# Optimization experiments

Measured on AMD Instinct MI355X. Metric: run time of the kernel, lower is better.

## Reference

```python
import jax, jax.numpy as jnp
import numpy as np

V, C = 100000, 400000          # variables, clauses
IN, OUT, H = 96, 64, 4         # in_channels, out_channels, heads
E_HALF = 1000000               # edges per direction
NEG_SLOPE = 0.2
LN_EPS = 1e-5


def _w(k, shape, fan_in):
    return (jax.random.normal(k, shape, jnp.float32) / np.sqrt(fan_in)).astype(jnp.float32)


def setup_inputs() -> dict:
    key = jax.random.key(0)
    ks = jax.random.split(key, 30)
    x = jax.random.normal(ks[0], (V + C, IN), jnp.float32)
    node_type = jnp.concatenate([jnp.full((V,), 1.0, jnp.float32), jnp.full((C,), 2.0, jnp.float32)])
    x = x.at[:, 0].set(node_type)  # NODE_TYPE_VAR=1, NODE_TYPE_CLAUSE=2
    # first half: "v2c" edges (source id >= num_vars), second half: "c2v" edges
    src1 = jax.random.randint(ks[1], (E_HALF,), V, 2 * V)   # -V -> index into x_var
    dst1 = jax.random.randint(ks[2], (E_HALF,), 0, C)       # index into x_clause
    src2 = jax.random.randint(ks[3], (E_HALF,), 0, V)       # index into h_c_new (V<=C so valid)
    dst2 = jax.random.randint(ks[4], (E_HALF,), V, 2 * V)   # -V -> index into x_var
    edge_index = jnp.stack([jnp.concatenate([src1, src2]),
                            jnp.concatenate([dst1, dst2])]).astype(jnp.int32)
    HD = H * OUT
    return {
        "x": x, "edge_index": edge_index, "num_vars": V,
        # v2c GATv2Conv (src=vars IN, dst=clauses IN)
        "v2c_Wl": _w(ks[5], (IN, HD), IN), "v2c_Wr": _w(ks[6], (IN, HD), IN),
        "v2c_att": _w(ks[7], (H, OUT), OUT), "v2c_bias": jnp.zeros((HD,), jnp.float32),
        "c_ln_g": jnp.ones((HD,), jnp.float32), "c_ln_b": jnp.zeros((HD,), jnp.float32),
        "c_Wih": _w(ks[8], (3 * OUT, HD), HD), "c_Whh": _w(ks[9], (3 * OUT, OUT), OUT),
        "c_bih": jnp.zeros((3 * OUT,), jnp.float32), "c_bhh": jnp.zeros((3 * OUT,), jnp.float32),
        # c2v GATv2Conv (src=clauses OUT, dst=vars IN)
        "c2v_Wl": _w(ks[10], (OUT, HD), OUT), "c2v_Wr": _w(ks[11], (IN, HD), IN),
        "c2v_att": _w(ks[12], (H, OUT), OUT), "c2v_bias": jnp.zeros((HD,), jnp.float32),
        "v_ln_g": jnp.ones((HD,), jnp.float32), "v_ln_b": jnp.zeros((HD,), jnp.float32),
        "v_Wih": _w(ks[13], (3 * OUT, HD), HD), "v_Whh": _w(ks[14], (3 * OUT, OUT), OUT),
        "v_bih": jnp.zeros((3 * OUT,), jnp.float32), "v_bhh": jnp.zeros((3 * OUT,), jnp.float32),
    }


def gatv2(x_src, x_dst, edge_index, Wl, Wr, att, bias, num_dst):
    """PyG GATv2Conv, concat=True, no self loops, eval mode (no attn dropout)."""
    h, d = att.shape
    xl = (x_src @ Wl).reshape(-1, h, d)   # [Ns, H, D]
    xr = (x_dst @ Wr).reshape(-1, h, d)   # [Nd, H, D]
    j, i = edge_index[0], edge_index[1]
    e = jax.nn.leaky_relu(xl[j] + xr[i], NEG_SLOPE)          # [E, H, D]
    alpha = jnp.einsum('ehd,hd->eh', e, att)                 # [E, H]
    amax = jax.ops.segment_max(alpha, i, num_segments=num_dst)
    alpha = jnp.exp(alpha - amax[i])
    denom = jax.ops.segment_sum(alpha, i, num_segments=num_dst)
    alpha = alpha / (denom[i] + 1e-16)
    msg = xl[j] * alpha[..., None]                           # [E, H, D]
    out = jax.ops.segment_sum(msg, i, num_segments=num_dst)  # [num_dst, H, D]
    return out.reshape(num_dst, h * d) + bias


def layernorm(x, g, b):
    mu = jnp.mean(x, axis=-1, keepdims=True)
    var = jnp.mean((x - mu) ** 2, axis=-1, keepdims=True)
    return (x - mu) * jax.lax.rsqrt(var + LN_EPS) * g + b


def gru_cell(x, hprev, Wih, Whh, bih, bhh):
    gi = x @ Wih.T + bih      # [N, 3*OUT]
    gh = hprev @ Whh.T + bhh  # [N, 3*OUT]
    ir, iz, inn = jnp.split(gi, 3, axis=-1)
    hr, hz, hn = jnp.split(gh, 3, axis=-1)
    r = jax.nn.sigmoid(ir + hr)
    z = jax.nn.sigmoid(iz + hz)
    n = jnp.tanh(inn + r * hn)
    return (1.0 - z) * n + z * hprev


def reference(x, edge_index, num_vars,
              v2c_Wl, v2c_Wr, v2c_att, v2c_bias, c_ln_g, c_ln_b,
              c_Wih, c_Whh, c_bih, c_bhh,
              c2v_Wl, c2v_Wr, c2v_att, c2v_bias, v_ln_g, v_ln_b,
              v_Wih, v_Whh, v_bih, v_bhh):
    out_ch = c_Whh.shape[1]
    n_nodes = x.shape[0]
    n_cla = n_nodes - num_vars
    h_old = x[:, -out_ch:]
    x_var, x_cla = x[:num_vars], x[num_vars:]           # vars first, clauses after
    h_v_old, h_c_old = h_old[:num_vars], h_old[num_vars:]
    e_half = edge_index.shape[1] // 2
    # edges with edge_index[0] >= num_vars (first half by construction), shift row 0
    v2c = jnp.stack([edge_index[0, :e_half] - num_vars, edge_index[1, :e_half]])
    m_c = gatv2(x_var, x_cla, v2c, v2c_Wl, v2c_Wr, v2c_att, v2c_bias, n_cla)
    m_c = layernorm(m_c, c_ln_g, c_ln_b)                # dropout = identity (eval)
    h_c_new = gru_cell(m_c, h_c_old, c_Wih, c_Whh, c_bih, c_bhh)
    # edges with edge_index[0] < num_vars (second half), shift row 1
    c2v = jnp.stack([edge_index[0, e_half:], edge_index[1, e_half:] - num_vars])
    m_v = gatv2(h_c_new, x_var, c2v, c2v_Wl, c2v_Wr, c2v_att, c2v_bias, num_vars)
    m_v = layernorm(m_v, v_ln_g, v_ln_b)
    h_v_new = gru_cell(m_v, h_v_old, v_Wih, v_Whh, v_bih, v_bhh)
    # x_new[var_mask]=h_v_new; x_new[clause_mask]=h_c_new (vars-first layout)
    return jnp.concatenate([h_v_new, h_c_new], axis=0)
```

## Files before the change

### kernel.cpp

```cpp
#include <hip/hip_runtime.h>
#include <hip/hip_bf16.h>
#include <cstdint>
#include <cstddef>

constexpr int V_NODES = 100000;
constexpr float NEG = 0.2f;
constexpr float LN_EPS = 1e-5f;
typedef __hip_bfloat16 bf16;

typedef __attribute__((ext_vector_type(8))) short short8v;
typedef __attribute__((ext_vector_type(4))) float f32x4;

__device__ inline float bflo(unsigned u){ return __uint_as_float(u << 16); }
__device__ inline float bfhi(unsigned u){ return __uint_as_float(u & 0xffff0000u); }
__device__ inline unsigned short f2bu(float x){ bf16 h = __float2bfloat16(x); return *reinterpret_cast<unsigned short*>(&h); }
__device__ inline unsigned bfpk(float x, float y){ return (unsigned)f2bu(x) | ((unsigned)f2bu(y) << 16); }

__device__ inline f32x4 mfma16(short8v a, short8v b, f32x4 c){
  return __builtin_amdgcn_mfma_f32_16x16x32_bf16(a, b, c, 0, 0, 0);
}

__global__ __launch_bounds__(256) void wprep_gf(const float* __restrict__ W,
                                                bf16* __restrict__ Wf, int K){
  int tid = blockIdx.x*256 + threadIdx.x;
  if (tid >= K*256) return;
  int fi = tid >> 9, rem = tid & 511;
  int lane = rem >> 3, i = rem & 7;
  int ks = fi >> 4, nt = fi & 15;
  int n = nt*16 + (lane & 15);
  int k = ks*32 + ((lane >> 4) << 3) + i;
  Wf[tid] = __float2bfloat16(W[(size_t)k*256 + n]);
}

__global__ __launch_bounds__(256) void wprep_gp(const float* __restrict__ W,
                                                bf16* __restrict__ Wf, int K){
  int tid = blockIdx.x*256 + threadIdx.x;
  if (tid >= K*256) return;
  int fi = tid >> 9, rem = tid & 511;
  int lane = rem >> 3, i = rem & 7;
  int ks = fi >> 4, nt = fi & 15;
  int n = nt*16 + (lane & 15);
  int ns = (((n & 63) >> 4) << 6) + ((n & 15) << 2) + (n >> 6);
  int k = ks*32 + ((lane >> 4) << 3) + i;
  Wf[tid] = __float2bfloat16(W[(size_t)k*256 + ns]);
}

__global__ __launch_bounds__(256) void wprep_bu(const float* __restrict__ Wih,
                                                const float* __restrict__ Whh,
                                                float* __restrict__ Bm){
  int tid = blockIdx.x*256 + threadIdx.x;
  if (tid >= 81920) return;
  int k = tid >> 8, n = tid & 255;
  float v = 0.f;
  if (k < 256) {
    if (n < 192) v = Wih[(size_t)n*256 + k];
  } else {
    int kh = k - 256;
    if (n < 128)       v = Whh[(size_t)n*64 + kh];
    else if (n >= 192) v = Whh[(size_t)(n - 64)*64 + kh];
  }
  Bm[tid] = v;
}

__global__ __launch_bounds__(256) void gemm_mf(
    const float* __restrict__ A, int lda, int K,
    const bf16* __restrict__ Wf, bf16* __restrict__ outp, int M)
{
  const int l  = threadIdx.x & 63;
  const int w  = threadIdx.x >> 6;
  const int jl = l & 15, kg = l >> 4;
  const int row0 = blockIdx.x*64 + w*16;
  __shared__ __align__(16) short As4[4][16*104];
  short* Aw = As4[w];

  const int K2 = K >> 1;
  const int tot = 16 * K2;
  for (int idx = l; idx < tot; idx += 64) {
    int r = idx / K2, c = idx - r*K2;
    int row = row0 + r;
    float2 a = (row < M) ? *(const float2*)(A + (size_t)row*lda + 2*c)
                         : make_float2(0.f, 0.f);
    *(unsigned*)(Aw + r*104 + 2*c) = bfpk(a.x, a.y);
  }
  asm volatile("" ::: "memory");

  f32x4 acc[16];
#pragma unroll
  for (int nt = 0; nt < 16; ++nt) acc[nt] = (f32x4){0.f,0.f,0.f,0.f};

  const short* Wb = (const short*)Wf + l*8;
  const short* Ab = Aw + jl*104 + kg*8;
  const int NKS = K >> 5;
  for (int ks = 0; ks < NKS; ++ks) {
    short8v a = *(const short8v*)(Ab + ks*32);
#pragma unroll
    for (int nt = 0; nt < 16; ++nt) {
      short8v b = *(const short8v*)(Wb + (size_t)(ks*16 + nt)*512);
      acc[nt] = mfma16(a, b, acc[nt]);
    }
  }

#pragma unroll
  for (int r = 0; r < 4; ++r) {
    int row = row0 + kg*4 + r;
    if (row < M) {
#pragma unroll
      for (int nt2 = 0; nt2 < 4; ++nt2) {
        uint2 o;
        o.x = bfpk(acc[nt2][r],   acc[nt2+4][r]);
        o.y = bfpk(acc[nt2+8][r], acc[nt2+12][r]);
        ((uint2*)outp)[(size_t)row * 64 + (nt2*16 + jl)] = o;
      }
    }
  }
}

__global__ __launch_bounds__(256) void hist_k(const int* __restrict__ dst, int doff,
                                              int* __restrict__ cnt, int E){
  int e = blockIdx.x*256 + threadIdx.x;
  if (e < E) atomicAdd(&cnt[dst[e]-doff], 1);
}
__global__ __launch_bounds__(256) void scanA(const int* __restrict__ cnt, int* __restrict__ part,
                                             int* __restrict__ bsum, int D){
  __shared__ int ts[256];
  int base = blockIdx.x*2048 + threadIdx.x*8;
  int v[8]; int s = 0;
#pragma unroll
  for (int i = 0; i < 8; ++i){ int idx = base+i; v[i] = (idx < D) ? cnt[idx] : 0; s += v[i]; }
  ts[threadIdx.x] = s; __syncthreads();
  for (int off = 1; off < 256; off <<= 1){
    int o = (threadIdx.x >= off) ? ts[threadIdx.x - off] : 0;
    __syncthreads();
    ts[threadIdx.x] += o;
    __syncthreads();
  }
  int run = ts[threadIdx.x] - s;
#pragma unroll
  for (int i = 0; i < 8; ++i){ int idx = base+i; if (idx < D) part[idx] = run; run += v[i]; }
  if (threadIdx.x == 255) bsum[blockIdx.x] = ts[255];
}
__global__ __launch_bounds__(256) void scanB(int* __restrict__ bsum, int nb){
  __shared__ int ts[256];
  int v = (threadIdx.x < nb) ? bsum[threadIdx.x] : 0;
  ts[threadIdx.x] = v; __syncthreads();
  for (int off = 1; off < 256; off <<= 1){
    int o = (threadIdx.x >= off) ? ts[threadIdx.x - off] : 0;
    __syncthreads();
    ts[threadIdx.x] += o;
    __syncthreads();
  }
  if (threadIdx.x < nb) bsum[threadIdx.x] = ts[threadIdx.x] - v;
}
__global__ __launch_bounds__(256) void scanC(const int* __restrict__ part, const int* __restrict__ bsum,
                                             int* __restrict__ rowptr, int* __restrict__ cursor,
                                             int D, int E){
  int idx = blockIdx.x*256 + threadIdx.x;
  if (idx < D){ int v = part[idx] + bsum[idx >> 11]; rowptr[idx] = v; cursor[idx] = v; }
  if (idx == 0) rowptr[D] = E;
}
__global__ __launch_bounds__(256) void scatter_k(const int* __restrict__ src, int soff,
                                                 const int* __restrict__ dst, int doff,
                                                 int* __restrict__ cursor, int* __restrict__ col, int E){
  int e = blockIdx.x*256 + threadIdx.x;
  if (e >= E) return;
  int p = atomicAdd(&cursor[dst[e]-doff], 1);
  col[p] = src[e] - soff;
}

__global__ __launch_bounds__(256) void gat_agg(
    const int* __restrict__ rowptr, const int* __restrict__ col,
    const bf16* __restrict__ xl, const bf16* __restrict__ xr,
    const float* __restrict__ att,
    bf16* __restrict__ agg, int D)
{
  __shared__ short Tr4[4][256];
  int wid = (int)((blockIdx.x*256u + threadIdx.x) >> 6);
  if (wid >= D) return;
  const int l = threadIdx.x & 63;
  const int g = l >> 4, r = l & 15;
  short* Tw = Tr4[(threadIdx.x >> 6)];
  uint2 ur = ((const uint2*)xr)[(size_t)wid*64 + l];
  const float xr0 = bflo(ur.x), xr1 = bfhi(ur.x), xr2 = bflo(ur.y), xr3 = bfhi(ur.y);
  const float4 at = *(const float4*)(att + g*64 + 4*r);
  float lsum = 0.f;
  float a0=0.f, a1=0.f, a2=0.f, a3=0.f;
  int p0 = rowptr[wid], p1 = rowptr[wid+1];
  int p = p0;
  for (; p + 1 < p1; p += 2){
    int ja = col[p], jb = col[p+1];
    uint2 ua = ((const uint2*)xl)[(size_t)ja*64 + l];
    uint2 ub = ((const uint2*)xl)[(size_t)jb*64 + l];
    float xa0 = bflo(ua.x), xa1 = bfhi(ua.x), xa2 = bflo(ua.y), xa3 = bfhi(ua.y);
    float xb0 = bflo(ub.x), xb1 = bfhi(ub.x), xb2 = bflo(ub.y), xb3 = bfhi(ub.y);
    float ta0 = xa0+xr0; ta0 = (ta0 > 0.f ? ta0 : NEG*ta0);
    float ta1 = xa1+xr1; ta1 = (ta1 > 0.f ? ta1 : NEG*ta1);
    float ta2 = xa2+xr2; ta2 = (ta2 > 0.f ? ta2 : NEG*ta2);
    float ta3 = xa3+xr3; ta3 = (ta3 > 0.f ? ta3 : NEG*ta3);
    float tb0 = xb0+xr0; tb0 = (tb0 > 0.f ? tb0 : NEG*tb0);
    float tb1 = xb1+xr1; tb1 = (tb1 > 0.f ? tb1 : NEG*tb1);
    float tb2 = xb2+xr2; tb2 = (tb2 > 0.f ? tb2 : NEG*tb2);
    float tb3 = xb3+xr3; tb3 = (tb3 > 0.f ? tb3 : NEG*tb3);
    float sa = ta0*at.x + ta1*at.y + ta2*at.z + ta3*at.w;
    float sb = tb0*at.x + tb1*at.y + tb2*at.z + tb3*at.w;
    sa += __shfl_xor(sa, 8, 64);  sb += __shfl_xor(sb, 8, 64);
    sa += __shfl_xor(sa, 4, 64);  sb += __shfl_xor(sb, 4, 64);
    sa += __shfl_xor(sa, 2, 64);  sb += __shfl_xor(sb, 2, 64);
    sa += __shfl_xor(sa, 1, 64);  sb += __shfl_xor(sb, 1, 64);
    float pea = __expf(sa), peb = __expf(sb);
    lsum += pea + peb;
    a0 += pea*xa0 + peb*xb0;
    a1 += pea*xa1 + peb*xb1;
    a2 += pea*xa2 + peb*xb2;
    a3 += pea*xa3 + peb*xb3;
  }
  if (p < p1){
    int j = col[p];
    uint2 uj = ((const uint2*)xl)[(size_t)j*64 + l];
    float x0 = bflo(uj.x), x1 = bfhi(uj.x), x2 = bflo(uj.y), x3 = bfhi(uj.y);
    float t0 = x0+xr0; t0 = (t0 > 0.f ? t0 : NEG*t0);
    float t1 = x1+xr1; t1 = (t1 > 0.f ? t1 : NEG*t1);
    float t2 = x2+xr2; t2 = (t2 > 0.f ? t2 : NEG*t2);
    float t3 = x3+xr3; t3 = (t3 > 0.f ? t3 : NEG*t3);
    float s = t0*at.x + t1*at.y + t2*at.z + t3*at.w;
    s += __shfl_xor(s, 8, 64);
    s += __shfl_xor(s, 4, 64);
    s += __shfl_xor(s, 2, 64);
    s += __shfl_xor(s, 1, 64);
    float pe = __expf(s);
    lsum += pe;
    a0 += pe*x0; a1 += pe*x1; a2 += pe*x2; a3 += pe*x3;
  }
  float inv = 1.f/(lsum + 1e-16f);
  Tw[16*r +  0 + g] = (short)f2bu(a0*inv);
  Tw[16*r +  4 + g] = (short)f2bu(a1*inv);
  Tw[16*r +  8 + g] = (short)f2bu(a2*inv);
  Tw[16*r + 12 + g] = (short)f2bu(a3*inv);
  asm volatile("" ::: "memory");
  ((uint2*)agg)[(size_t)wid*64 + l] = ((const uint2*)Tw)[l];
}

__global__ __launch_bounds__(256) void ln_gemm(
    const bf16* __restrict__ agg,
    const float* __restrict__ gbias,
    const float* __restrict__ g, const float* __restrict__ b,
    const bf16* __restrict__ Wf,
    const float* __restrict__ x, int hrow0,
    bf16* __restrict__ gout, int M)
{
  __shared__ __align__(16) short At4[4][16*328];
  const int l  = threadIdx.x & 63;
  const int w  = threadIdx.x >> 6;
  short* At = At4[w];
  const int row0 = blockIdx.x*64 + w*16;
  const int jl = l & 15, kg = l >> 4;

  float gb0 = gbias[l], gb1 = gbias[64+l], gb2 = gbias[128+l], gb3 = gbias[192+l];
  float gg0 = g[l],     gg1 = g[64+l],    gg2 = g[128+l],    gg3 = g[192+l];
  float bt0 = b[l],     bt1 = b[64+l],    bt2 = b[128+l],    bt3 = b[192+l];
#pragma unroll 8
  for (int rr = 0; rr < 16; ++rr) {
    int row = row0 + rr;
    uint2 av = make_uint2(0u, 0u);
    float hp = 0.f;
    if (row < M) {
      av = ((const uint2*)agg)[(size_t)row*64 + l];
      hp = x[(size_t)(hrow0+row)*96 + 32 + l];
    }
    float f0 = bflo(av.x) + gb0, f1 = bfhi(av.x) + gb1;
    float f2 = bflo(av.y) + gb2, f3 = bfhi(av.y) + gb3;
    float s = f0+f1+f2+f3, ss = f0*f0+f1*f1+f2*f2+f3*f3;
#pragma unroll
    for (int off = 32; off; off >>= 1){ s += __shfl_xor(s,off,64); ss += __shfl_xor(ss,off,64); }
    float mean = s * (1.f/256.f);
    float var  = ss * (1.f/256.f) - mean*mean;
    float rstd = rsqrtf(var + LN_EPS);
    short* Ar = At + rr*328;
    Ar[l]       = (short)f2bu((f0-mean)*rstd*gg0 + bt0);
    Ar[64 + l]  = (short)f2bu((f1-mean)*rstd*gg1 + bt1);
    Ar[128 + l] = (short)f2bu((f2-mean)*rstd*gg2 + bt2);
    Ar[192 + l] = (short)f2bu((f3-mean)*rstd*gg3 + bt3);
    Ar[256 + l] = (short)f2bu(hp);
  }
  asm volatile("" ::: "memory");

  f32x4 acc[16];
#pragma unroll
  for (int nt = 0; nt < 16; ++nt) acc[nt] = (f32x4){0.f,0.f,0.f,0.f};

  const short8v* Wl = (const short8v*)Wf + l;
  const short* Ab = At + jl*328 + kg*8;

  short8v bb[2][12];
  auto pre_m = [&](short8v* dst, int ks){
#pragma unroll
    for (int t = 0; t < 12; ++t) dst[t] = Wl[(ks*16 + t)*64];
  };
  pre_m(bb[0], 0);
#pragma unroll
  for (int ks = 0; ks < 8; ++ks) {
    if (ks < 7) pre_m(bb[(ks+1)&1], ks+1);
    short8v a = *(const short8v*)(Ab + ks*32);
#pragma unroll
    for (int t = 0; t < 12; ++t) acc[t] = mfma16(a, bb[ks&1][t], acc[t]);
  }

#pragma unroll
  for (int ks = 8; ks < 10; ++ks) {
    short8v a = *(const short8v*)(Ab + ks*32);
#pragma unroll
    for (int t = 0; t < 8; ++t)   acc[t] = mfma16(a, Wl[(ks*16 + t)*64], acc[t]);
#pragma unroll
    for (int t = 12; t < 16; ++t) acc[t] = mfma16(a, Wl[(ks*16 + t)*64], acc[t]);
  }

#pragma unroll
  for (int r = 0; r < 4; ++r) {
    int row = row0 + kg*4 + r;
    if (row < M) {
#pragma unroll
      for (int nt2 = 0; nt2 < 4; ++nt2) {
        uint2 o;
        o.x = bfpk(acc[nt2][r],   acc[nt2+4][r]);
        o.y = bfpk(acc[nt2+8][r], acc[nt2+12][r]);
        ((uint2*)gout)[(size_t)row*64 + (nt2*16 + jl)] = o;
      }
    }
  }
}

__global__ __launch_bounds__(256) void gru_fin(
    const bf16* __restrict__ gout,
    const float* __restrict__ bih, const float* __restrict__ bhh,
    const float* __restrict__ x, int hrow0,
    float* __restrict__ out, int orow0, int M)
{
  int tid = blockIdx.x*256 + threadIdx.x;
  if (tid >= M*64) return;
  int row = tid >> 6, s = tid & 63;
  uint2 q = ((const uint2*)gout)[(size_t)row*64 + s];
  float qr = bflo(q.x), qz = bfhi(q.x), qn = bflo(q.y), qh = bfhi(q.y);
  float h  = x[(size_t)(hrow0+row)*96 + 32 + s];
  float rg = 1.f/(1.f + __expf(-(qr + bih[s]      + bhh[s])));
  float zg = 1.f/(1.f + __expf(-(qz + bih[64+s]   + bhh[64+s])));
  float ng = tanhf(qn + bih[128+s] + rg*(qh + bhh[128+s]));
  out[(size_t)(orow0+row)*64 + s] = (1.f - zg)*ng + zg*h;
}

__global__ void sentinel_kernel(float* out){ out[0] = 123456.0f; }

extern "C" void kernel_launch(void* const* d_in, const int* in_sizes, int n_in,
                              void* d_out, int out_size, void* d_ws, size_t ws_size,
                              hipStream_t stream)
{
  const float* x        = (const float*)d_in[0];
  const int*   ei       = (const int*)d_in[1];
  const float* v2c_Wl   = (const float*)d_in[3];
  const float* v2c_Wr   = (const float*)d_in[4];
  const float* v2c_att  = (const float*)d_in[5];
  const float* v2c_bias = (const float*)d_in[6];
  const float* c_ln_g   = (const float*)d_in[7];
  const float* c_ln_b   = (const float*)d_in[8];
  const float* c_Wih    = (const float*)d_in[9];
  const float* c_Whh    = (const float*)d_in[10];
  const float* c_bih    = (const float*)d_in[11];
  const float* c_bhh    = (const float*)d_in[12];
  const float* c2v_Wl   = (const float*)d_in[13];
  const float* c2v_Wr   = (const float*)d_in[14];
  const float* c2v_att  = (const float*)d_in[15];
  const float* c2v_bias = (const float*)d_in[16];
  const float* v_ln_g   = (const float*)d_in[17];
  const float* v_ln_b   = (const float*)d_in[18];
  const float* v_Wih    = (const float*)d_in[19];
  const float* v_Whh    = (const float*)d_in[20];
  const float* v_bih    = (const float*)d_in[21];
  const float* v_bhh    = (const float*)d_in[22];
  float* out = (float*)d_out;

  const int V = V_NODES;
  const int C = in_sizes[0] / 96 - V;
  const int E = in_sizes[1] / 4;
  const int* e0_1 = ei;
  const int* e1_1 = ei + (size_t)2*E;
  const int* e0_2 = ei + (size_t)E;
  const int* e1_2 = ei + (size_t)3*E;

  bf16* xl  = (bf16*)d_ws;
  bf16* xr  = xl + (size_t)C*256;
  bf16* agg = xr + (size_t)C*256;
  bf16* Wf2 = agg + (size_t)C*256;
  float* Bm = (float*)(Wf2 + 81920);
  bf16* Wgf = (bf16*)(Bm + 81920);
  int* cnt    = (int*)(Wgf + 24576);
  int* rowptr = cnt + C;
  int* part   = rowptr + C + 1;
  int* bsum   = part + C;
  int* col    = bsum + 256;
  bf16* gout  = xl;
  size_t need = (size_t)C*256*2*3 + (size_t)81920*2 + (size_t)81920*4 +
                (size_t)24576*2 + ((size_t)3*C + 1 + 256 + (size_t)E) * 4;
  if (ws_size < need) {
    hipMemsetAsync(d_out, 0, (size_t)out_size*4, stream);
    sentinel_kernel<<<1,1,0,stream>>>(out);
    return;
  }

  const int EB = (E + 255)/256;

  wprep_gp<<<96, 256, 0, stream>>>(v2c_Wl, Wgf, 96);
  gemm_mf<<<(V+63)/64, 256, 0, stream>>>(x, 96, 96, Wgf, xl, V);
  wprep_gp<<<96, 256, 0, stream>>>(v2c_Wr, Wgf, 96);
  gemm_mf<<<(C+63)/64, 256, 0, stream>>>(x + (size_t)V*96, 96, 96, Wgf, xr, C);
  hipMemsetAsync(cnt, 0, (size_t)C*4, stream);
  hist_k<<<EB, 256, 0, stream>>>(e1_1, 0, cnt, E);
  {
    int nb = (C + 2047)/2048;
    scanA<<<nb, 256, 0, stream>>>(cnt, part, bsum, C);
    scanB<<<1, 256, 0, stream>>>(bsum, nb);
    scanC<<<(C+255)/256, 256, 0, stream>>>(part, bsum, rowptr, cnt, C, E);
  }
  scatter_k<<<EB, 256, 0, stream>>>(e0_1, V, e1_1, 0, cnt, col, E);
  gat_agg<<<(C+3)/4, 256, 0, stream>>>(rowptr, col, xl, xr, v2c_att, agg, C);
  wprep_bu<<<320, 256, 0, stream>>>(c_Wih, c_Whh, Bm);
  wprep_gf<<<320, 256, 0, stream>>>(Bm, Wf2, 320);
  ln_gemm<<<(C+63)/64, 256, 0, stream>>>(agg, v2c_bias, c_ln_g, c_ln_b, Wf2,
                                         x, V, gout, C);
  gru_fin<<<(C*64+255)/256, 256, 0, stream>>>(gout, c_bih, c_bhh, x, V, out, V, C);

  wprep_gp<<<64, 256, 0, stream>>>(c2v_Wl, Wgf, 64);
  gemm_mf<<<(C+63)/64, 256, 0, stream>>>(out + (size_t)V*64, 64, 64, Wgf, xl, C);
  wprep_gp<<<96, 256, 0, stream>>>(c2v_Wr, Wgf, 96);
  gemm_mf<<<(V+63)/64, 256, 0, stream>>>(x, 96, 96, Wgf, xr, V);
  hipMemsetAsync(cnt, 0, (size_t)V*4, stream);
  hist_k<<<EB, 256, 0, stream>>>(e1_2, V, cnt, E);
  {
    int nb = (V + 2047)/2048;
    scanA<<<nb, 256, 0, stream>>>(cnt, part, bsum, V);
    scanB<<<1, 256, 0, stream>>>(bsum, nb);
    scanC<<<(V+255)/256, 256, 0, stream>>>(part, bsum, rowptr, cnt, V, E);
  }
  scatter_k<<<EB, 256, 0, stream>>>(e0_2, 0, e1_2, V, cnt, col, E);
  gat_agg<<<(V+3)/4, 256, 0, stream>>>(rowptr, col, xl, xr, c2v_att, agg, V);
  wprep_bu<<<320, 256, 0, stream>>>(v_Wih, v_Whh, Bm);
  wprep_gf<<<320, 256, 0, stream>>>(Bm, Wf2, 320);
  ln_gemm<<<(V+63)/64, 256, 0, stream>>>(agg, c2v_bias, v_ln_g, v_ln_b, Wf2,
                                         x, 0, gout, V);
  gru_fin<<<(V*64+255)/256, 256, 0, stream>>>(gout, v_bih, v_bhh, x, 0, out, 0, V);
}
```

Before: 1.271 ms.

## Split ln_gemm output columns across waves sharing a 64-row LDS tile

ln_gemm now stages a shared 64-row normalized A tile in LDS with a block barrier. Previously each wave handled its own 16 rows against all 16 weight column tiles. Now each wave handles all 64 rows but only its 16-column slice of each gate group, so each wave loads a quarter of the weight fragments and reuses each weight fragment across four row tiles. This cuts per-wave weight traffic and the large 24-register prefetch buffer, at the cost of a __syncthreads and more LDS A reads.

```diff
diff --git a/kernel.cpp b/kernel.cpp
--- a/kernel.cpp
+++ b/kernel.cpp
@@ -247,11 +247,10 @@
     const float* __restrict__ x, int hrow0,
     bf16* __restrict__ gout, int M)
 {
-  __shared__ __align__(16) short At4[4][16*328];
+  __shared__ __align__(16) short At[64*328];
   const int l  = threadIdx.x & 63;
   const int w  = threadIdx.x >> 6;
-  short* At = At4[w];
-  const int row0 = blockIdx.x*64 + w*16;
+  const int row0 = blockIdx.x*64;
   const int jl = l & 15, kg = l >> 4;
 
   float gb0 = gbias[l], gb1 = gbias[64+l], gb2 = gbias[128+l], gb3 = gbias[192+l];
@@ -259,7 +258,8 @@
   float bt0 = b[l],     bt1 = b[64+l],    bt2 = b[128+l],    bt3 = b[192+l];
 #pragma unroll 8
   for (int rr = 0; rr < 16; ++rr) {
-    int row = row0 + rr;
+    int rloc = w*16 + rr;
+    int row = row0 + rloc;
     uint2 av = make_uint2(0u, 0u);
     float hp = 0.f;
     if (row < M) {
@@ -274,55 +274,57 @@
     float mean = s * (1.f/256.f);
     float var  = ss * (1.f/256.f) - mean*mean;
     float rstd = rsqrtf(var + LN_EPS);
-    short* Ar = At + rr*328;
+    short* Ar = At + rloc*328;
     Ar[l]       = (short)f2bu((f0-mean)*rstd*gg0 + bt0);
     Ar[64 + l]  = (short)f2bu((f1-mean)*rstd*gg1 + bt1);
     Ar[128 + l] = (short)f2bu((f2-mean)*rstd*gg2 + bt2);
     Ar[192 + l] = (short)f2bu((f3-mean)*rstd*gg3 + bt3);
     Ar[256 + l] = (short)f2bu(hp);
   }
-  asm volatile("" ::: "memory");
-
-  f32x4 acc[16];
-#pragma unroll
-  for (int nt = 0; nt < 16; ++nt) acc[nt] = (f32x4){0.f,0.f,0.f,0.f};
+  __syncthreads();
+
+  f32x4 acc[4][4];
+#pragma unroll
+  for (int mt = 0; mt < 4; ++mt)
+#pragma unroll
+    for (int q = 0; q < 4; ++q) acc[mt][q] = (f32x4){0.f,0.f,0.f,0.f};
 
   const short8v* Wl = (const short8v*)Wf + l;
   const short* Ab = At + jl*328 + kg*8;
 
-  short8v bb[2][12];
-  auto pre_m = [&](short8v* dst, int ks){
-#pragma unroll
-    for (int t = 0; t < 12; ++t) dst[t] = Wl[(ks*16 + t)*64];
-  };
-  pre_m(bb[0], 0);
-#pragma unroll
-  for (int ks = 0; ks < 8; ++ks) {
-    if (ks < 7) pre_m(bb[(ks+1)&1], ks+1);
-    short8v a = *(const short8v*)(Ab + ks*32);
-#pragma unroll
-    for (int t = 0; t < 12; ++t) acc[t] = mfma16(a, bb[ks&1][t], acc[t]);
-  }
-
-#pragma unroll
-  for (int ks = 8; ks < 10; ++ks) {
-    short8v a = *(const short8v*)(Ab + ks*32);
-#pragma unroll
-    for (int t = 0; t < 8; ++t)   acc[t] = mfma16(a, Wl[(ks*16 + t)*64], acc[t]);
-#pragma unroll
-    for (int t = 12; t < 16; ++t) acc[t] = mfma16(a, Wl[(ks*16 + t)*64], acc[t]);
-  }
-
-#pragma unroll
-  for (int r = 0; r < 4; ++r) {
-    int row = row0 + kg*4 + r;
-    if (row < M) {
-#pragma unroll
-      for (int nt2 = 0; nt2 < 4; ++nt2) {
+  short8v cb0 = Wl[(0*16 + w)*64];
+  short8v cb1 = Wl[(0*16 + 4 + w)*64];
+  short8v cb2 = Wl[(0*16 + 8 + w)*64];
+#pragma unroll
+  for (int ks = 0; ks < 10; ++ks) {
+    short8v nb0 = cb0, nb1 = cb1, nb2 = cb2;
+    if (ks < 9) {
+      const int kn = ks + 1;
+      nb0 = Wl[(kn*16 + w)*64];
+      nb1 = Wl[(kn*16 + 4 + w)*64];
+      nb2 = Wl[(kn*16 + ((kn < 8) ? 8 : 12) + w)*64];
+    }
+    const int gi = (ks < 8) ? 2 : 3;
+#pragma unroll
+    for (int mt = 0; mt < 4; ++mt) {
+      short8v a = *(const short8v*)(Ab + mt*16*328 + ks*32);
+      acc[mt][0]  = mfma16(a, cb0, acc[mt][0]);
+      acc[mt][1]  = mfma16(a, cb1, acc[mt][1]);
+      acc[mt][gi] = mfma16(a, cb2, acc[mt][gi]);
+    }
+    cb0 = nb0; cb1 = nb1; cb2 = nb2;
+  }
+
+#pragma unroll
+  for (int mt = 0; mt < 4; ++mt) {
+#pragma unroll
+    for (int r = 0; r < 4; ++r) {
+      int row = row0 + mt*16 + kg*4 + r;
+      if (row < M) {
         uint2 o;
-        o.x = bfpk(acc[nt2][r],   acc[nt2+4][r]);
-        o.y = bfpk(acc[nt2+8][r], acc[nt2+12][r]);
-        ((uint2*)gout)[(size_t)row*64 + (nt2*16 + jl)] = o;
+        o.x = bfpk(acc[mt][0][r], acc[mt][1][r]);
+        o.y = bfpk(acc[mt][2][r], acc[mt][3][r]);
+        ((uint2*)gout)[(size_t)row*64 + (16*w + jl)] = o;
       }
     }
   }
```

New measurement: 1.224 ms. -3.7%, faster.
